# Kernel tuning notes

Measured on AMD Instinct MI355X. Metric: run time of the kernel, lower is better.

The kernel has to match this reference:

```python
import jax, jax.numpy as jnp
import numpy as np

# Dimensions: S=Scount nodes, R=Rcount(=n_classes), B=len(source_index)
S, R, IN_F, OUT_F, H, B, C = 10000, 16, 128, 128, 4, 2048, 16
NEG = -9e15


def _bn(x, g, b):
    # BatchNorm1d, training-mode batch statistics (biased var), eps=1e-5
    m = x.mean(0)
    v = x.var(0)
    return (x - m) / jnp.sqrt(v + 1e-5) * g + b


def setup_inputs() -> dict:
    key = jax.random.key(0)
    ks = jax.random.split(key, 13)
    n = lambda k, s: jax.random.normal(k, s, jnp.float32) * 0.1
    return {
        "inter_adj": jax.random.randint(ks[0], (S, R), 0, 2, jnp.int32),
        "city_adj": jax.random.randint(ks[1], (S, S), 0, 2, jnp.int32),
        "province_adj": jax.random.randint(ks[2], (S, S), 0, 2, jnp.int32),
        "source_index": jax.random.randint(ks[3], (B,), 0, S, jnp.int32),
        "Sfeat": n(ks[4], (S, IN_F)),
        "Rfeat": n(ks[5], (R, IN_F)),
        "W1": n(ks[6], (H, IN_F, OUT_F)),
        "W2": n(ks[7], (H, IN_F, OUT_F)),
        "a": n(ks[8], (H, 2 * OUT_F)),
        "a3": n(ks[9], (H, 2 * OUT_F)),
        "a4": n(ks[10], (H, 2 * OUT_F)),
        "bn1_g": jnp.ones((H, OUT_F), jnp.float32),
        "bn1_b": jnp.zeros((H, OUT_F), jnp.float32),
        "bn2_g": jnp.ones((H, OUT_F), jnp.float32),
        "bn2_b": jnp.zeros((H, OUT_F), jnp.float32),
        "outW": n(ks[11], (H * R, C)),
        "outA": n(ks[12], (2 * C,)),
    }


def _forward(inter_adj, city_adj, province_adj, src, Sfeat, Rfeat,
             W1, W2, a, a3, a4, bn1_g, bn1_b, bn2_g, bn2_b, outW, outA):
    Fd = OUT_F
    inter_m = inter_adj > 0            # [S, R]
    city_m = city_adj[src] > 0         # [B, S]
    prov_m = province_adj[src] > 0     # [B, S]
    # Dropout is identity (eval mode); the concat+matmul attention scores are
    # computed as separable rank-1 terms instead of materializing O(S*R*2F).

    def head(W1h, W2h, ah, a3h, a4h, g1h, b1h, g2h, b2h):
        h1 = Rfeat @ W1h               # [R, F]
        h2 = Sfeat @ W2h               # [S, F]
        h2s = h2[src]                  # [B, F]
        # e12[i,j] = lrelu(a[:F].h1[j] + a[F:].h2[i])
        e12 = jax.nn.leaky_relu((h2 @ ah[Fd:])[:, None] + (h1 @ ah[:Fd])[None, :], 0.2)
        att_i = jax.nn.softmax(jnp.where(inter_m, e12, NEG), axis=1)   # [S, R]
        # cat([h3, h3]) -> score constant over the neighbor axis
        e3 = jax.nn.leaky_relu(h2s @ (a3h[:Fd] + a3h[Fd:]), 0.2)[:, None]  # [B,1]
        att3 = jax.nn.softmax(jnp.where(city_m, e3, NEG), axis=1)      # [B, S]
        e4 = jax.nn.leaky_relu(h2s @ (a4h[:Fd] + a4h[Fd:]), 0.2)[:, None]
        att4 = jax.nn.softmax(jnp.where(prov_m, e4, NEG), axis=1)
        InterRC = att_i @ h1                        # [S, F]
        IntraNC = (att3 + att4).T @ h2s             # [S, F]
        v = jax.nn.leaky_relu(_bn(att_i.T @ h2, g1h, b1h), 0.2)  # [R, F]
        u = jax.nn.leaky_relu(_bn(InterRC + IntraNC, g2h, b2h), 0.2)  # [S, F]
        return jax.nn.elu(u @ v.T)                  # [S, R]

    hx = jax.vmap(head)(W1, W2, a, a3, a4, bn1_g, bn1_b, bn2_g, bn2_b)  # [H,S,R]
    x = jnp.transpose(hx, (1, 0, 2)).reshape(S, H * R)
    # output GraphAttentionLayer
    h = x @ outW                                    # [S, C]
    e = jax.nn.leaky_relu(h @ (outA[:C] + outA[C:]), 0.2)[:, None]  # [S,1]
    att = jax.nn.softmax(jnp.where(inter_m, jnp.broadcast_to(e, inter_m.shape), NEG), axis=1)
    # elu inside layer, then elu again in ablation2, then log_softmax
    return jax.nn.log_softmax(jax.nn.elu(jax.nn.elu(att * h)), axis=1)


def reference(inter_adj, city_adj, province_adj, source_index, Sfeat, Rfeat,
              W1, W2, a, a3, a4, bn1_g, bn1_b, bn2_g, bn2_b, outW, outA):
    return _forward(inter_adj, city_adj, province_adj, source_index, Sfeat, Rfeat,
                    W1, W2, a, a3, a4, bn1_g, bn1_b, bn2_g, bn2_b, outW, outA)
```

## Files before the change

### kernel.cpp

```cpp
#include <hip/hip_runtime.h>
#include <hip/hip_bf16.h>
#include <stdint.h>

#define S_N 10000
#define MPAD 10112
#define B_N 2048
#define F_N 128

typedef __bf16 bf16x8 __attribute__((ext_vector_type(8)));
typedef __bf16 bf16x4 __attribute__((ext_vector_type(4)));
typedef float  f32x4  __attribute__((ext_vector_type(4)));
typedef unsigned long long u64;
typedef unsigned int u32;
typedef unsigned short u16;

union Bf8 { u16 us[8]; bf16x8 v; };
union Bh8 { __bf16 h[8]; bf16x8 v; };

__device__ __forceinline__ float lrelu02(float x) { return x >= 0.0f ? x : 0.2f * x; }
__device__ __forceinline__ float eluf(float x)    { return x > 0.0f ? x : expm1f(x); }

__global__ __launch_bounds__(256) void k_bits_pre(const int* __restrict__ adj_c,
        const int* __restrict__ adj_p, const int* __restrict__ src,
        const float* __restrict__ Sfeat, const float* __restrict__ Rfeat,
        const float* __restrict__ W1, const float* __restrict__ W2, const float* __restrict__ a,
        u64* __restrict__ tcity, u64* __restrict__ tprov,
        u32* __restrict__ cc, u32* __restrict__ pc,
        __bf16* __restrict__ SfB, __bf16* __restrict__ W2T, __bf16* __restrict__ h1T,
        float* __restrict__ q) {
    const int bid = blockIdx.x, t = threadIdx.x;
    if (bid < 1280) {
        const int sc = bid % 20, wb = (bid / 20) % 32, mat = bid / 640;
        const int l = t & 63, w = t >> 6;
        const int* adj = mat ? adj_p : adj_c;
        u64* tb = mat ? tprov : tcity;
        u32* cnt = mat ? pc : cc;
        __shared__ u64 wt[64][8];
        __shared__ u32 lc[64];
        if (t < 64) lc[t] = 0;
        __syncthreads();
        const int s1 = sc * 512 + t;
        const int s2 = s1 + 256;
        for (int bb = 0; bb < 64; ++bb) {
            int row = src[wb * 64 + bb];
            const int* rp = adj + (size_t)row * S_N;
            int v1 = (s1 < S_N) ? rp[s1] : 0;
            int v2 = (s2 < S_N) ? rp[s2] : 0;
            u64 b1 = __ballot(v1 > 0);
            u64 b2 = __ballot(v2 > 0);
            if (l == 0) {
                wt[bb][w] = b1;
                wt[bb][w + 4] = b2;
                atomicAdd(&lc[bb], (u32)(__popcll(b1) + __popcll(b2)));
            }
        }
        __syncthreads();
        if (t < 64) atomicAdd(&cnt[wb * 64 + t], lc[t]);
        for (int tile = w; tile < 8; tile += 4) {
            u64 wv = wt[l][tile];
            u64 myw = 0;
            #pragma unroll
            for (int j = 0; j < 64; ++j) {
                u64 bal = __ballot((int)((wv >> j) & 1ull));
                if (l == j) myw = bal;
            }
            int s = sc * 512 + tile * 64 + l;
            if (s < MPAD) tb[(size_t)wb * MPAD + s] = myw;
        }
    } else if (bid < 6336) {
        int i = (bid - 1280) * 256 + t;
        int s = i >> 7;
        SfB[i] = (__bf16)(s < S_N ? Sfeat[i] : 0.0f);
    } else if (bid < 6592) {
        int idx = (bid - 6336) * 256 + t;
        int hn = idx >> 7, k = idx & 127;
        int h = hn >> 7, n = hn & 127;
        W2T[idx] = (__bf16)W2[(h * F_N + k) * F_N + n];
    } else {
        __shared__ float red[256];
        int b2i = bid - 6592;
        int h = b2i >> 4, r = b2i & 15;
        float hv = 0.0f;
        if (t < 128) {
            const float* rf = Rfeat + r * F_N;
            const float* wp = W1 + h * F_N * F_N + t;
            for (int k = 0; k < F_N; ++k) hv += rf[k] * wp[k * F_N];
        }
        red[t] = (t < 128) ? hv * a[h * 256 + t] : 0.0f;
        __syncthreads();
        for (int off = 128; off > 0; off >>= 1) {
            if (t < off) red[t] += red[t + off];
            __syncthreads();
        }
        if (t == 0) q[h * 16 + r] = red[0];
        if (t < 128) {
            h1T[(h * F_N + t) * 32 + r] = (__bf16)hv;
            h1T[(h * F_N + t) * 32 + 16 + r] = (__bf16)0.0f;
        }
    }
}

__global__ __launch_bounds__(256) void k_yz(const float* __restrict__ Sfeat,
        const int* __restrict__ src, const u32* __restrict__ cc, const u32* __restrict__ pc,
        __bf16* __restrict__ YT, __bf16* __restrict__ ZT) {
    int idx = blockIdx.x * 256 + threadIdx.x;
    int f = idx >> 11, b = idx & 2047;
    float sv = Sfeat[src[b] * F_N + f];
    float icc = cc[b] ? 1.0f / (float)cc[b] : 0.0f;
    float ipc = pc[b] ? 1.0f / (float)pc[b] : 0.0f;
    YT[f * B_N + b] = (__bf16)(sv * icc);
    ZT[f * B_N + b] = (__bf16)(sv * ipc);
}

__global__ __launch_bounds__(256) void g_T(const __bf16* __restrict__ YT, const __bf16* __restrict__ ZT,
        const u64* __restrict__ tcity, const u64* __restrict__ tprov, float* __restrict__ Tp) {
    const int t = threadIdx.x, l = t & 63, w = t >> 6;
    const int wm = w >> 1, wn = w & 1;
    const int quad = l >> 4, ln = l & 15;
    const int s_blk = blockIdx.x * 128;
    const unsigned char* cb = (const unsigned char*)tcity;
    const unsigned char* pb = (const unsigned char*)tprov;
    const f32x4 fz = {0.0f, 0.0f, 0.0f, 0.0f};
    f32x4 acc[4][4];
    #pragma unroll
    for (int mt = 0; mt < 4; ++mt)
        #pragma unroll
        for (int nt = 0; nt < 4; ++nt) acc[mt][nt] = fz;
    const int k_base = blockIdx.y * 512;
    for (int it = 0; it < 16; ++it) {
        int kk = k_base + it * 32;
        bf16x8 Ya[4], Za[4];
        #pragma unroll
        for (int mt = 0; mt < 4; ++mt) {
            int f = wm * 64 + mt * 16 + ln;
            Ya[mt] = *(const bf16x8*)(YT + f * B_N + kk + quad * 8);
            Za[mt] = *(const bf16x8*)(ZT + f * B_N + kk + quad * 8);
        }
        bf16x8 Bc[4], Bp[4];
        #pragma unroll
        for (int nt = 0; nt < 4; ++nt) {
            int s = s_blk + wn * 64 + nt * 16 + ln;
            size_t base = ((size_t)(kk >> 6) * MPAD + s) * 8 + ((kk >> 3) & 7) + quad;
            unsigned int cby = cb[base], pby = pb[base];
            Bf8 uc, up;
            #pragma unroll
            for (int j = 0; j < 8; ++j) {
                uc.us[j] = ((cby >> j) & 1u) ? (u16)0x3F80 : (u16)0;
                up.us[j] = ((pby >> j) & 1u) ? (u16)0x3F80 : (u16)0;
            }
            Bc[nt] = uc.v; Bp[nt] = up.v;
        }
        #pragma unroll
        for (int mt = 0; mt < 4; ++mt)
            #pragma unroll
            for (int nt = 0; nt < 4; ++nt) {
                acc[mt][nt] = __builtin_amdgcn_mfma_f32_16x16x32_bf16(Ya[mt], Bc[nt], acc[mt][nt], 0, 0, 0);
                acc[mt][nt] = __builtin_amdgcn_mfma_f32_16x16x32_bf16(Za[mt], Bp[nt], acc[mt][nt], 0, 0, 0);
            }
    }
    float* tp = Tp + (size_t)blockIdx.y * ((size_t)MPAD * F_N);
    #pragma unroll
    for (int nt = 0; nt < 4; ++nt) {
        int s = s_blk + wn * 64 + nt * 16 + ln;
        #pragma unroll
        for (int mt = 0; mt < 4; ++mt) {
            int f0 = wm * 64 + mt * 16 + quad * 4;
            *(f32x4*)(tp + (size_t)s * F_N + f0) = acc[mt][nt];
        }
    }
}

__global__ __launch_bounds__(256) void k_tred(const float* __restrict__ Tp, __bf16* __restrict__ Tb) {
    int i4 = blockIdx.x * 256 + threadIdx.x;
    size_t base = (size_t)i4 * 4;
    const size_t stride = (size_t)MPAD * F_N;
    f32x4 s0 = *(const f32x4*)(Tp + base);
    f32x4 s1 = *(const f32x4*)(Tp + stride + base);
    f32x4 s2 = *(const f32x4*)(Tp + 2 * stride + base);
    f32x4 s3 = *(const f32x4*)(Tp + 3 * stride + base);
    f32x4 sum = s0 + s1 + s2 + s3;
    bf16x4 o;
    #pragma unroll
    for (int j = 0; j < 4; ++j) o[j] = (__bf16)sum[j];
    *(bf16x4*)(Tb + base) = o;
}

__global__ __launch_bounds__(256) void g_h2attM(const __bf16* __restrict__ A, const __bf16* __restrict__ W2T,
        const float* __restrict__ a, const float* __restrict__ q, const int* __restrict__ inter,
        __bf16* __restrict__ attb, float* __restrict__ Mg) {
    const int t = threadIdx.x, l = t & 63, w = t >> 6;
    const int wm = w >> 1, wn = w & 1, quad = l >> 4, ln = l & 15;
    const int s0 = blockIdx.x * 128, h = blockIdx.y;
    __shared__ __bf16 h2T[128 * 136];
    __shared__ __bf16 attT[16 * 136];
    __shared__ float ps[128];
    if (t < 128) ps[t] = 0.0f;
    __syncthreads();
    const f32x4 fz = {0.0f, 0.0f, 0.0f, 0.0f};
    f32x4 acc[4][4];
    #pragma unroll
    for (int mt = 0; mt < 4; ++mt)
        #pragma unroll
        for (int nt = 0; nt < 4; ++nt) acc[mt][nt] = fz;
    #pragma unroll
    for (int it = 0; it < 4; ++it) {
        int kk = it * 32;
        bf16x8 af[4], bfr[4];
        #pragma unroll
        for (int mt = 0; mt < 4; ++mt)
            af[mt] = *(const bf16x8*)(A + (size_t)(s0 + wm * 64 + mt * 16 + ln) * F_N + kk + quad * 8);
        #pragma unroll
        for (int nt = 0; nt < 4; ++nt)
            bfr[nt] = *(const bf16x8*)(W2T + (size_t)(h * F_N + wn * 64 + nt * 16 + ln) * F_N + kk + quad * 8);
        #pragma unroll
        for (int mt = 0; mt < 4; ++mt)
            #pragma unroll
            for (int nt = 0; nt < 4; ++nt)
                acc[mt][nt] = __builtin_amdgcn_mfma_f32_16x16x32_bf16(af[mt], bfr[nt], acc[mt][nt], 0, 0, 0);
    }
    float a2v[4];
    #pragma unroll
    for (int nt = 0; nt < 4; ++nt) a2v[nt] = a[h * 256 + 128 + wn * 64 + nt * 16 + ln];
    #pragma unroll
    for (int mt = 0; mt < 4; ++mt) {
        #pragma unroll
        for (int nt = 0; nt < 4; ++nt) {
            bf16x4 o;
            #pragma unroll
            for (int j = 0; j < 4; ++j) o[j] = (__bf16)acc[mt][nt][j];
            *(bf16x4*)(&h2T[(wn * 64 + nt * 16 + ln) * 136 + wm * 64 + mt * 16 + quad * 4]) = o;
        }
        #pragma unroll
        for (int r = 0; r < 4; ++r) {
            float pp = 0.0f;
            #pragma unroll
            for (int nt = 0; nt < 4; ++nt) pp += acc[mt][nt][r] * a2v[nt];
            #pragma unroll
            for (int m = 8; m > 0; m >>= 1) pp += __shfl_xor(pp, m, 16);
            if (ln == 0) atomicAdd(&ps[wm * 64 + mt * 16 + quad * 4 + r], pp);
        }
    }
    __syncthreads();
    if (t < 128) {
        int s = s0 + t;
        if (s < S_N) {
            float pv = ps[t];
            float e[16];
            int msk[16], cn = 0;
            float mx = -3e38f;
            #pragma unroll
            for (int c = 0; c < 16; ++c) {
                msk[c] = inter[s * 16 + c] > 0;
                cn += msk[c];
                e[c] = lrelu02(pv + q[h * 16 + c]);
                if (msk[c]) mx = fmaxf(mx, e[c]);
            }
            float sm = 0.0f;
            #pragma unroll
            for (int c = 0; c < 16; ++c) {
                e[c] = msk[c] ? expf(e[c] - mx) : 0.0f;
                sm += e[c];
            }
            float inv = cn > 0 ? 1.0f / sm : 0.0f;
            #pragma unroll
            for (int c = 0; c < 16; ++c) {
                float av = cn > 0 ? e[c] * inv : 0.0625f;
                attb[((size_t)h * MPAD + s) * 16 + c] = (__bf16)av;
                attT[c * 136 + t] = (__bf16)av;
            }
        } else {
            #pragma unroll
            for (int c = 0; c < 16; ++c) {
                attb[((size_t)h * MPAD + s) * 16 + c] = (__bf16)0.0f;
                attT[c * 136 + t] = (__bf16)0.0f;
            }
        }
    }
    __syncthreads();
    #pragma unroll
    for (int fi = 0; fi < 2; ++fi) {
        int ft = 2 * w + fi;
        f32x4 macc = fz;
        #pragma unroll
        for (int kit = 0; kit < 4; ++kit) {
            bf16x8 av = *(const bf16x8*)(&attT[ln * 136 + kit * 32 + quad * 8]);
            bf16x8 bv = *(const bf16x8*)(&h2T[(ft * 16 + ln) * 136 + kit * 32 + quad * 8]);
            macc = __builtin_amdgcn_mfma_f32_16x16x32_bf16(av, bv, macc, 0, 0, 0);
        }
        #pragma unroll
        for (int r = 0; r < 4; ++r)
            atomicAdd(&Mg[(h * 16 + quad * 4 + r) * F_N + ft * 16 + ln], macc[r]);
    }
}

__global__ __launch_bounds__(256) void g_P(const __bf16* __restrict__ Tb, const __bf16* __restrict__ W2T,
        const __bf16* __restrict__ attb, const __bf16* __restrict__ h1T,
        float* __restrict__ P, float* __restrict__ usum, float* __restrict__ usq) {
    const int t = threadIdx.x, l = t & 63, w = t >> 6;
    const int wm = w >> 1, wn = w & 1, quad = l >> 4, ln = l & 15;
    const int s0 = blockIdx.x * 128, h = blockIdx.y;
    const f32x4 fz = {0.0f, 0.0f, 0.0f, 0.0f};
    f32x4 acc[4][4];
    #pragma unroll
    for (int mt = 0; mt < 4; ++mt)
        #pragma unroll
        for (int nt = 0; nt < 4; ++nt) acc[mt][nt] = fz;
    {
        bf16x8 a2[4], b2[4];
        #pragma unroll
        for (int mt = 0; mt < 4; ++mt) {
            int s = s0 + wm * 64 + mt * 16 + ln;
            Bf8 az;
            az.v = *(const bf16x8*)(attb + ((size_t)h * MPAD + s) * 16 + (quad & 1) * 8);
            if (quad >= 2) {
                #pragma unroll
                for (int j = 0; j < 8; ++j) az.us[j] = 0;
            }
            a2[mt] = az.v;
        }
        #pragma unroll
        for (int nt = 0; nt < 4; ++nt) {
            int f = wn * 64 + nt * 16 + ln;
            b2[nt] = *(const bf16x8*)(h1T + ((size_t)(h * F_N + f)) * 32 + quad * 8);
        }
        #pragma unroll
        for (int mt = 0; mt < 4; ++mt)
            #pragma unroll
            for (int nt = 0; nt < 4; ++nt)
                acc[mt][nt] = __builtin_amdgcn_mfma_f32_16x16x32_bf16(a2[mt], b2[nt], acc[mt][nt], 0, 0, 0);
    }
    #pragma unroll
    for (int it = 0; it < 4; ++it) {
        int kk = it * 32;
        bf16x8 af[4], bfr[4];
        #pragma unroll
        for (int mt = 0; mt < 4; ++mt)
            af[mt] = *(const bf16x8*)(Tb + (size_t)(s0 + wm * 64 + mt * 16 + ln) * F_N + kk + quad * 8);
        #pragma unroll
        for (int nt = 0; nt < 4; ++nt)
            bfr[nt] = *(const bf16x8*)(W2T + (size_t)(h * F_N + wn * 64 + nt * 16 + ln) * F_N + kk + quad * 8);
        #pragma unroll
        for (int mt = 0; mt < 4; ++mt)
            #pragma unroll
            for (int nt = 0; nt < 4; ++nt)
                acc[mt][nt] = __builtin_amdgcn_mfma_f32_16x16x32_bf16(af[mt], bfr[nt], acc[mt][nt], 0, 0, 0);
    }
    __shared__ float lsum[128], lsq[128];
    if (t < 128) { lsum[t] = 0.0f; lsq[t] = 0.0f; }
    __syncthreads();
    #pragma unroll
    for (int nt = 0; nt < 4; ++nt) {
        int f = wn * 64 + nt * 16 + ln;
        float p1 = 0.0f, p2 = 0.0f;
        #pragma unroll
        for (int mt = 0; mt < 4; ++mt) {
            int sb = s0 + wm * 64 + mt * 16 + quad * 4;
            #pragma unroll
            for (int r = 0; r < 4; ++r) {
                float val = acc[mt][nt][r];
                P[((size_t)h * MPAD + sb + r) * F_N + f] = val;
                p1 += val; p2 += val * val;
            }
        }
        atomicAdd(&lsum[f], p1);
        atomicAdd(&lsq[f], p2);
    }
    __syncthreads();
    if (t < 128) {
        atomicAdd(&usum[h * F_N + t], lsum[t]);
        atomicAdd(&usq[h * F_N + t], lsq[t]);
    }
}

__global__ __launch_bounds__(256) void g_out(const float* __restrict__ P,
        const float* __restrict__ usum, const float* __restrict__ usq, const float* __restrict__ Mg,
        const float* __restrict__ g1, const float* __restrict__ b1,
        const float* __restrict__ g2, const float* __restrict__ b2,
        const float* __restrict__ outW, const int* __restrict__ inter, float* __restrict__ out) {
    const int t = threadIdx.x, l = t & 63, w = t >> 6, quad = l >> 4, ln = l & 15;
    const int s0 = blockIdx.x * 64;
    __shared__ __bf16 v_lds[64 * 136];
    __shared__ float G_lds[64 * 68];
    __shared__ float scs[512], shs[512];
    __shared__ float W_lds[1024];
    for (int i = t; i < 1024; i += 256) W_lds[i] = outW[i];
    if (t < 128) {
        #pragma unroll
        for (int h = 0; h < 4; ++h) {
            int i = h * F_N + t;
            float mean = usum[i] * (1.0f / S_N);
            float var = usq[i] * (1.0f / S_N) - mean * mean;
            float sc = g2[i] * rsqrtf(var + 1e-5f);
            scs[i] = sc;
            shs[i] = b2[i] - mean * sc;
        }
    }
    {
        int f = t & 127;
        int hb = (t >> 7) * 2;
        #pragma unroll
        for (int hh = hb; hh < hb + 2; ++hh) {
            float mv[16], s1 = 0.0f, s2 = 0.0f;
            #pragma unroll
            for (int r = 0; r < 16; ++r) {
                mv[r] = Mg[(hh * 16 + r) * F_N + f];
                s1 += mv[r]; s2 += mv[r] * mv[r];
            }
            float m1 = s1 * 0.0625f, v1 = s2 * 0.0625f - m1 * m1;
            int i = hh * F_N + f;
            float g = g1[i] * rsqrtf(v1 + 1e-5f);
            float bb = b1[i] - m1 * g;
            #pragma unroll
            for (int r = 0; r < 16; ++r)
                v_lds[(hh * 16 + r) * 136 + f] = (__bf16)lrelu02(mv[r] * g + bb);
        }
    }
    __syncthreads();
    const int h = w;
    const f32x4 fz = {0.0f, 0.0f, 0.0f, 0.0f};
    #pragma unroll
    for (int mt = 0; mt < 4; ++mt) {
        f32x4 gacc = fz;
        int s = s0 + mt * 16 + ln;
        #pragma unroll
        for (int kit = 0; kit < 4; ++kit) {
            int k0 = kit * 32 + quad * 8;
            const float* pp = P + ((size_t)h * MPAD + s) * F_N + k0;
            f32x4 p0 = *(const f32x4*)pp;
            f32x4 p1 = *(const f32x4*)(pp + 4);
            f32x4 c0 = *(const f32x4*)(scs + h * F_N + k0);
            f32x4 c1 = *(const f32x4*)(scs + h * F_N + k0 + 4);
            f32x4 d0 = *(const f32x4*)(shs + h * F_N + k0);
            f32x4 d1 = *(const f32x4*)(shs + h * F_N + k0 + 4);
            Bh8 af;
            #pragma unroll
            for (int j = 0; j < 4; ++j) {
                af.h[j]     = (__bf16)lrelu02(p0[j] * c0[j] + d0[j]);
                af.h[j + 4] = (__bf16)lrelu02(p1[j] * c1[j] + d1[j]);
            }
            bf16x8 bv = *(const bf16x8*)(&v_lds[(h * 16 + ln) * 136 + k0]);
            gacc = __builtin_amdgcn_mfma_f32_16x16x32_bf16(af.v, bv, gacc, 0, 0, 0);
        }
        #pragma unroll
        for (int r = 0; r < 4; ++r)
            G_lds[(mt * 16 + quad * 4 + r) * 68 + h * 16 + ln] = eluf(gacc[r]);
    }
    __syncthreads();
    const int c = t & 15, ss = t >> 4;
    #pragma unroll
    for (int pass = 0; pass < 4; ++pass) {
        int sl = pass * 16 + ss;
        int s = s0 + sl;
        float hm = 0.0f;
        #pragma unroll
        for (int j = 0; j < 64; ++j) hm += G_lds[sl * 68 + j] * W_lds[j * 16 + c];
        int valid = s < S_N;
        int msk = valid ? (inter[(valid ? s : 0) * 16 + c] > 0) : 0;
        int cn = msk;
        #pragma unroll
        for (int m = 8; m > 0; m >>= 1) cn += __shfl_xor(cn, m, 16);
        float attf = cn > 0 ? (msk ? 1.0f / (float)cn : 0.0f) : 0.0625f;
        float y = eluf(eluf(attf * hm));
        float mx = y;
        #pragma unroll
        for (int m = 8; m > 0; m >>= 1) mx = fmaxf(mx, __shfl_xor(mx, m, 16));
        float ex = expf(y - mx);
        float sm = ex;
        #pragma unroll
        for (int m = 8; m > 0; m >>= 1) sm += __shfl_xor(sm, m, 16);
        if (valid) out[s * 16 + c] = y - mx - logf(sm);
    }
}

extern "C" void kernel_launch(void* const* d_in, const int* in_sizes, int n_in,
                              void* d_out, int out_size, void* d_ws, size_t ws_size,
                              hipStream_t stream) {
    const int* inter = (const int*)d_in[0];
    const int* city  = (const int*)d_in[1];
    const int* prov  = (const int*)d_in[2];
    const int* src   = (const int*)d_in[3];
    const float* Sfeat = (const float*)d_in[4];
    const float* Rfeat = (const float*)d_in[5];
    const float* W1 = (const float*)d_in[6];
    const float* W2 = (const float*)d_in[7];
    const float* a  = (const float*)d_in[8];
    const float* g1 = (const float*)d_in[11];
    const float* b1 = (const float*)d_in[12];
    const float* g2 = (const float*)d_in[13];
    const float* b2 = (const float*)d_in[14];
    const float* outW = (const float*)d_in[15];
    float* out = (float*)d_out;

    char* p = (char*)d_ws;
    float* M    = (float*)p; p += 4 * 16 * F_N * 4;
    float* usum = (float*)p; p += 2048;
    float* usq  = (float*)p; p += 2048;
    u32*   cc   = (u32*)p;   p += 8192;
    u32*   pc   = (u32*)p;   p += 8192;
    size_t zbytes = (size_t)(p - (char*)d_ws);
    u64* tcity = (u64*)p; p += 32 * (size_t)MPAD * 8;
    u64* tprov = (u64*)p; p += 32 * (size_t)MPAD * 8;
    __bf16* YT  = (__bf16*)p; p += (size_t)F_N * B_N * 2;
    __bf16* ZT  = (__bf16*)p; p += (size_t)F_N * B_N * 2;
    __bf16* SfB = (__bf16*)p; p += (size_t)MPAD * F_N * 2;
    __bf16* W2T = (__bf16*)p; p += 512 * 128 * 2;
    __bf16* h1T = (__bf16*)p; p += 4 * 128 * 32 * 2;
    float*  q   = (float*)p;  p += 512;
    float*  Tp  = (float*)p;  p += 4 * (size_t)MPAD * F_N * 4;
    __bf16* Tb  = (__bf16*)p; p += (size_t)MPAD * F_N * 2;
    __bf16* attb= (__bf16*)p; p += 4 * (size_t)MPAD * 16 * 2;
    float*  P   = (float*)p;  p += 4 * (size_t)MPAD * F_N * 4;

    hipMemsetAsync(d_ws, 0, zbytes, stream);
    k_bits_pre<<<6656, 256, 0, stream>>>(city, prov, src, Sfeat, Rfeat, W1, W2, a,
                                         tcity, tprov, cc, pc, SfB, W2T, h1T, q);
    k_yz      <<<1024, 256, 0, stream>>>(Sfeat, src, cc, pc, YT, ZT);
    g_T       <<<dim3(79, 4), 256, 0, stream>>>(YT, ZT, tcity, tprov, Tp);
    k_tred    <<<1264, 256, 0, stream>>>(Tp, Tb);
    g_h2attM  <<<dim3(79, 4), 256, 0, stream>>>(SfB, W2T, a, q, inter, attb, M);
    g_P       <<<dim3(79, 4), 256, 0, stream>>>(Tb, W2T, attb, h1T, P, usum, usq);
    g_out     <<<157, 256, 0, stream>>>(P, usum, usq, M, g1, b1, g2, b2, outW, inter, out);
}
```

Baseline: 791.1 us.

## Fuse split-K reduction into g_T and merge attention and P kernels

The split-K reduction of T moves into g_T: the last-arriving block for each row tile (tracked with an atomic ticket counter) sums the four partials and writes the bf16 result. g_h2attM and g_P are merged into a single g_mid kernel that keeps the attention weights in LDS rather than writing and re-reading them from global memory. P is now stored as bf16 instead of fp32, and g_out processes 32 rows per block across twice as many blocks. This cuts two launches and a good deal of global traffic, in exchange for a threadfence-based inter-block handoff, more LDS per block, and reduced precision in the intermediate P.

```diff
diff --git a/kernel.cpp b/kernel.cpp
--- a/kernel.cpp
+++ b/kernel.cpp
@@ -113,7 +113,8 @@
 }
 
 __global__ __launch_bounds__(256) void g_T(const __bf16* __restrict__ YT, const __bf16* __restrict__ ZT,
-        const u64* __restrict__ tcity, const u64* __restrict__ tprov, float* __restrict__ Tp) {
+        const u64* __restrict__ tcity, const u64* __restrict__ tprov,
+        float* __restrict__ Tp, u32* __restrict__ tick, __bf16* __restrict__ Tb) {
     const int t = threadIdx.x, l = t & 63, w = t >> 6;
     const int wm = w >> 1, wn = w & 1;
     const int quad = l >> 4, ln = l & 15;
@@ -168,33 +169,47 @@
             *(f32x4*)(tp + (size_t)s * F_N + f0) = acc[mt][nt];
         }
     }
+    __shared__ u32 lastv;
+    __syncthreads();
+    if (t == 0) {
+        __threadfence();
+        lastv = atomicAdd(&tick[blockIdx.x], 1u);
+    }
+    __syncthreads();
+    if (lastv == 3u) {
+        __threadfence();
+        const size_t stride = (size_t)MPAD * F_N;
+        for (int idx = t; idx < 4096; idx += 256) {
+            size_t off = (size_t)s_blk * F_N + (size_t)idx * 4;
+            f32x4 v0 = *(const f32x4*)(Tp + off);
+            f32x4 v1 = *(const f32x4*)(Tp + stride + off);
+            f32x4 v2 = *(const f32x4*)(Tp + 2 * stride + off);
+            f32x4 v3 = *(const f32x4*)(Tp + 3 * stride + off);
+            f32x4 sum = v0 + v1 + v2 + v3;
+            bf16x4 o;
+            #pragma unroll
+            for (int j = 0; j < 4; ++j) o[j] = (__bf16)sum[j];
+            *(bf16x4*)(Tb + off) = o;
+        }
+    }
 }
 
-__global__ __launch_bounds__(256) void k_tred(const float* __restrict__ Tp, __bf16* __restrict__ Tb) {
-    int i4 = blockIdx.x * 256 + threadIdx.x;
-    size_t base = (size_t)i4 * 4;
-    const size_t stride = (size_t)MPAD * F_N;
-    f32x4 s0 = *(const f32x4*)(Tp + base);
-    f32x4 s1 = *(const f32x4*)(Tp + stride + base);
-    f32x4 s2 = *(const f32x4*)(Tp + 2 * stride + base);
-    f32x4 s3 = *(const f32x4*)(Tp + 3 * stride + base);
-    f32x4 sum = s0 + s1 + s2 + s3;
-    bf16x4 o;
-    #pragma unroll
-    for (int j = 0; j < 4; ++j) o[j] = (__bf16)sum[j];
-    *(bf16x4*)(Tb + base) = o;
-}
-
-__global__ __launch_bounds__(256) void g_h2attM(const __bf16* __restrict__ A, const __bf16* __restrict__ W2T,
+__global__ __launch_bounds__(256) void g_mid(const __bf16* __restrict__ A, const __bf16* __restrict__ W2T,
+        const __bf16* __restrict__ Tb, const __bf16* __restrict__ h1T,
         const float* __restrict__ a, const float* __restrict__ q, const int* __restrict__ inter,
-        __bf16* __restrict__ attb, float* __restrict__ Mg) {
+        float* __restrict__ Mg, float* __restrict__ usum, float* __restrict__ usq,
+        __bf16* __restrict__ P) {
     const int t = threadIdx.x, l = t & 63, w = t >> 6;
     const int wm = w >> 1, wn = w & 1, quad = l >> 4, ln = l & 15;
     const int s0 = blockIdx.x * 128, h = blockIdx.y;
     __shared__ __bf16 h2T[128 * 136];
     __shared__ __bf16 attT[16 * 136];
+    __shared__ __bf16 attN[128 * 32];
     __shared__ float ps[128];
-    if (t < 128) ps[t] = 0.0f;
+    __shared__ float lsum[128], lsq[128];
+    if (t < 128) { ps[t] = 0.0f; lsum[t] = 0.0f; lsq[t] = 0.0f; }
+    #pragma unroll
+    for (int i = t; i < 128 * 32; i += 256) attN[i] = (__bf16)0.0f;
     __syncthreads();
     const f32x4 fz = {0.0f, 0.0f, 0.0f, 0.0f};
     f32x4 acc[4][4];
@@ -265,15 +280,12 @@
             #pragma unroll
             for (int c = 0; c < 16; ++c) {
                 float av = cn > 0 ? e[c] * inv : 0.0625f;
-                attb[((size_t)h * MPAD + s) * 16 + c] = (__bf16)av;
+                attN[t * 32 + c] = (__bf16)av;
                 attT[c * 136 + t] = (__bf16)av;
             }
         } else {
             #pragma unroll
-            for (int c = 0; c < 16; ++c) {
-                attb[((size_t)h * MPAD + s) * 16 + c] = (__bf16)0.0f;
-                attT[c * 136 + t] = (__bf16)0.0f;
-            }
+            for (int c = 0; c < 16; ++c) attT[c * 136 + t] = (__bf16)0.0f;
         }
     }
     __syncthreads();
@@ -291,16 +303,6 @@
         for (int r = 0; r < 4; ++r)
             atomicAdd(&Mg[(h * 16 + quad * 4 + r) * F_N + ft * 16 + ln], macc[r]);
     }
-}
-
-__global__ __launch_bounds__(256) void g_P(const __bf16* __restrict__ Tb, const __bf16* __restrict__ W2T,
-        const __bf16* __restrict__ attb, const __bf16* __restrict__ h1T,
-        float* __restrict__ P, float* __restrict__ usum, float* __restrict__ usq) {
-    const int t = threadIdx.x, l = t & 63, w = t >> 6;
-    const int wm = w >> 1, wn = w & 1, quad = l >> 4, ln = l & 15;
-    const int s0 = blockIdx.x * 128, h = blockIdx.y;
-    const f32x4 fz = {0.0f, 0.0f, 0.0f, 0.0f};
-    f32x4 acc[4][4];
     #pragma unroll
     for (int mt = 0; mt < 4; ++mt)
         #pragma unroll
@@ -309,14 +311,8 @@
         bf16x8 a2[4], b2[4];
         #pragma unroll
         for (int mt = 0; mt < 4; ++mt) {
-            int s = s0 + wm * 64 + mt * 16 + ln;
-            Bf8 az;
-            az.v = *(const bf16x8*)(attb + ((size_t)h * MPAD + s) * 16 + (quad & 1) * 8);
-            if (quad >= 2) {
-                #pragma unroll
-                for (int j = 0; j < 8; ++j) az.us[j] = 0;
-            }
-            a2[mt] = az.v;
+            int sl = wm * 64 + mt * 16 + ln;
+            a2[mt] = *(const bf16x8*)(&attN[sl * 32 + quad * 8]);
         }
         #pragma unroll
         for (int nt = 0; nt < 4; ++nt) {
@@ -345,8 +341,6 @@
             for (int nt = 0; nt < 4; ++nt)
                 acc[mt][nt] = __builtin_amdgcn_mfma_f32_16x16x32_bf16(af[mt], bfr[nt], acc[mt][nt], 0, 0, 0);
     }
-    __shared__ float lsum[128], lsq[128];
-    if (t < 128) { lsum[t] = 0.0f; lsq[t] = 0.0f; }
     __syncthreads();
     #pragma unroll
     for (int nt = 0; nt < 4; ++nt) {
@@ -354,11 +348,11 @@
         float p1 = 0.0f, p2 = 0.0f;
         #pragma unroll
         for (int mt = 0; mt < 4; ++mt) {
-            int sb = s0 + wm * 64 + mt * 16 + quad * 4;
+            int sb = wm * 64 + mt * 16 + quad * 4;
             #pragma unroll
             for (int r = 0; r < 4; ++r) {
                 float val = acc[mt][nt][r];
-                P[((size_t)h * MPAD + sb + r) * F_N + f] = val;
+                h2T[(sb + r) * 136 + f] = (__bf16)val;
                 p1 += val; p2 += val * val;
             }
         }
@@ -370,17 +364,22 @@
         atomicAdd(&usum[h * F_N + t], lsum[t]);
         atomicAdd(&usq[h * F_N + t], lsq[t]);
     }
+    for (int g = t; g < 2048; g += 256) {
+        int sl = g >> 4, fg = (g & 15) * 8;
+        bf16x8 v = *(const bf16x8*)(&h2T[sl * 136 + fg]);
+        *(bf16x8*)(P + ((size_t)h * MPAD + s0 + sl) * F_N + fg) = v;
+    }
 }
 
-__global__ __launch_bounds__(256) void g_out(const float* __restrict__ P,
+__global__ __launch_bounds__(256) void g_out(const __bf16* __restrict__ P,
         const float* __restrict__ usum, const float* __restrict__ usq, const float* __restrict__ Mg,
         const float* __restrict__ g1, const float* __restrict__ b1,
         const float* __restrict__ g2, const float* __restrict__ b2,
         const float* __restrict__ outW, const int* __restrict__ inter, float* __restrict__ out) {
     const int t = threadIdx.x, l = t & 63, w = t >> 6, quad = l >> 4, ln = l & 15;
-    const int s0 = blockIdx.x * 64;
+    const int s0 = blockIdx.x * 32;
     __shared__ __bf16 v_lds[64 * 136];
-    __shared__ float G_lds[64 * 68];
+    __shared__ float G_lds[32 * 68];
     __shared__ float scs[512], shs[512];
     __shared__ float W_lds[1024];
     for (int i = t; i < 1024; i += 256) W_lds[i] = outW[i];
@@ -400,13 +399,13 @@
         int hb = (t >> 7) * 2;
         #pragma unroll
         for (int hh = hb; hh < hb + 2; ++hh) {
-            float mv[16], s1 = 0.0f, s2 = 0.0f;
+            float mv[16], sa = 0.0f, sb = 0.0f;
             #pragma unroll
             for (int r = 0; r < 16; ++r) {
                 mv[r] = Mg[(hh * 16 + r) * F_N + f];
-                s1 += mv[r]; s2 += mv[r] * mv[r];
-            }
-            float m1 = s1 * 0.0625f, v1 = s2 * 0.0625f - m1 * m1;
+                sa += mv[r]; sb += mv[r] * mv[r];
+            }
+            float m1 = sa * 0.0625f, v1 = sb * 0.0625f - m1 * m1;
             int i = hh * F_N + f;
             float g = g1[i] * rsqrtf(v1 + 1e-5f);
             float bb = b1[i] - m1 * g;
@@ -419,24 +418,18 @@
     const int h = w;
     const f32x4 fz = {0.0f, 0.0f, 0.0f, 0.0f};
     #pragma unroll
-    for (int mt = 0; mt < 4; ++mt) {
+    for (int mt = 0; mt < 2; ++mt) {
         f32x4 gacc = fz;
         int s = s0 + mt * 16 + ln;
         #pragma unroll
         for (int kit = 0; kit < 4; ++kit) {
             int k0 = kit * 32 + quad * 8;
-            const float* pp = P + ((size_t)h * MPAD + s) * F_N + k0;
-            f32x4 p0 = *(const f32x4*)pp;
-            f32x4 p1 = *(const f32x4*)(pp + 4);
-            f32x4 c0 = *(const f32x4*)(scs + h * F_N + k0);
-            f32x4 c1 = *(const f32x4*)(scs + h * F_N + k0 + 4);
-            f32x4 d0 = *(const f32x4*)(shs + h * F_N + k0);
-            f32x4 d1 = *(const f32x4*)(shs + h * F_N + k0 + 4);
+            bf16x8 pv = *(const bf16x8*)(P + ((size_t)h * MPAD + s) * F_N + k0);
             Bh8 af;
             #pragma unroll
-            for (int j = 0; j < 4; ++j) {
-                af.h[j]     = (__bf16)lrelu02(p0[j] * c0[j] + d0[j]);
-                af.h[j + 4] = (__bf16)lrelu02(p1[j] * c1[j] + d1[j]);
+            for (int j = 0; j < 8; ++j) {
+                int f = k0 + j;
+                af.h[j] = (__bf16)lrelu02((float)pv[j] * scs[h * F_N + f] + shs[h * F_N + f]);
             }
             bf16x8 bv = *(const bf16x8*)(&v_lds[(h * 16 + ln) * 136 + k0]);
             gacc = __builtin_amdgcn_mfma_f32_16x16x32_bf16(af.v, bv, gacc, 0, 0, 0);
@@ -448,7 +441,7 @@
     __syncthreads();
     const int c = t & 15, ss = t >> 4;
     #pragma unroll
-    for (int pass = 0; pass < 4; ++pass) {
+    for (int pass = 0; pass < 2; ++pass) {
         int sl = pass * 16 + ss;
         int s = s0 + sl;
         float hm = 0.0f;
@@ -497,6 +490,7 @@
     float* usq  = (float*)p; p += 2048;
     u32*   cc   = (u32*)p;   p += 8192;
     u32*   pc   = (u32*)p;   p += 8192;
+    u32*   tick = (u32*)p;   p += 512;
     size_t zbytes = (size_t)(p - (char*)d_ws);
     u64* tcity = (u64*)p; p += 32 * (size_t)MPAD * 8;
     u64* tprov = (u64*)p; p += 32 * (size_t)MPAD * 8;
@@ -508,16 +502,13 @@
     float*  q   = (float*)p;  p += 512;
     float*  Tp  = (float*)p;  p += 4 * (size_t)MPAD * F_N * 4;
     __bf16* Tb  = (__bf16*)p; p += (size_t)MPAD * F_N * 2;
-    __bf16* attb= (__bf16*)p; p += 4 * (size_t)MPAD * 16 * 2;
-    float*  P   = (float*)p;  p += 4 * (size_t)MPAD * F_N * 4;
+    __bf16* P   = (__bf16*)p; p += 4 * (size_t)MPAD * F_N * 2;
 
     hipMemsetAsync(d_ws, 0, zbytes, stream);
     k_bits_pre<<<6656, 256, 0, stream>>>(city, prov, src, Sfeat, Rfeat, W1, W2, a,
                                          tcity, tprov, cc, pc, SfB, W2T, h1T, q);
     k_yz      <<<1024, 256, 0, stream>>>(Sfeat, src, cc, pc, YT, ZT);
-    g_T       <<<dim3(79, 4), 256, 0, stream>>>(YT, ZT, tcity, tprov, Tp);
-    k_tred    <<<1264, 256, 0, stream>>>(Tp, Tb);
-    g_h2attM  <<<dim3(79, 4), 256, 0, stream>>>(SfB, W2T, a, q, inter, attb, M);
-    g_P       <<<dim3(79, 4), 256, 0, stream>>>(Tb, W2T, attb, h1T, P, usum, usq);
-    g_out     <<<157, 256, 0, stream>>>(P, usum, usq, M, g1, b1, g2, b2, outW, inter, out);
+    g_T       <<<dim3(79, 4), 256, 0, stream>>>(YT, ZT, tcity, tprov, Tp, tick, Tb);
+    g_mid     <<<dim3(79, 4), 256, 0, stream>>>(SfB, W2T, Tb, h1T, a, q, inter, M, usum, usq, P);
+    g_out     <<<316, 256, 0, stream>>>(P, usum, usq, M, g1, b1, g2, b2, outW, inter, out);
 }
```

After: 802.8 us. About the same (+1.5%).
